# Kernel optimization log

Measured on AMD Instinct MI355X. Metric: run time of the kernel, lower is better.

Reference implementation:

```python
import jax, jax.numpy as jnp
import numpy as np
import itertools

EPS = 1e-5
SCALE = 16 ** -0.5  # key_dim ** -0.5
H_HEADS, KEY_DIM, D, RES, RES_, STRIDE = 8, 16, 32, 28, 14, 2


def hardswish(x):
    return x * jnp.clip(x + 3.0, 0.0, 6.0) / 6.0


def conv_bn_hw(x, w, g, b, m, v):
    # 1x1 conv (no bias) + eval-mode BatchNorm + Hardswish
    y = jnp.einsum('bchw,oc->bohw', x, w)
    scale = (g / jnp.sqrt(v + EPS))[:, None, None]
    y = (y - m[:, None, None]) * scale + b[:, None, None]
    return hardswish(y)


def _bias_idxs():
    offsets, idxs = {}, []
    for p1 in itertools.product(range(RES_), repeat=2):
        for p2 in itertools.product(range(RES), repeat=2):
            off = (abs(p1[0] * STRIDE - p2[0]), abs(p1[1] * STRIDE - p2[1]))
            if off not in offsets:
                offsets[off] = len(offsets)
            idxs.append(offsets[off])
    return np.array(idxs, dtype=np.int32).reshape(RES_ * RES_, RES * RES), len(offsets)


def setup_inputs() -> dict:
    key = jax.random.key(0)
    ks = jax.random.split(key, 8)
    B, C = 64, 256
    idxs, n_off = _bias_idxs()

    def bn_params(k, n):
        k1, k2, k3, k4 = jax.random.split(k, 4)
        return (jax.random.normal(k1, (n,)) * 0.1 + 1.0,
                jax.random.normal(k2, (n,)) * 0.1,
                jax.random.normal(k3, (n,)) * 0.1,
                jax.random.uniform(k4, (n,), minval=0.5, maxval=1.5))

    kv_g, kv_b, kv_m, kv_v = bn_params(ks[1], 384)
    q_g, q_b, q_m, q_v = bn_params(ks[2], 128)
    p_g, p_b, p_m, p_v = bn_params(ks[3], 512)
    return dict(
        x=jax.random.normal(ks[0], (B, C, 28, 28), dtype=jnp.float32),
        kv_w=jax.random.normal(ks[4], (384, C)) * 0.05,
        kv_g=kv_g, kv_b=kv_b, kv_m=kv_m, kv_v=kv_v,
        q_w=jax.random.normal(ks[5], (128, C)) * 0.05,
        q_g=q_g, q_b=q_b, q_m=q_m, q_v=q_v,
        proj_w=jax.random.normal(ks[6], (512, 256)) * 0.05,
        proj_g=p_g, proj_b=p_b, proj_m=p_m, proj_v=p_v,
        ab=jax.random.normal(ks[7], (H_HEADS, n_off)) * 0.02,
        bias_idxs=jnp.asarray(idxs),
    )


def reference(x, kv_w, kv_g, kv_b, kv_m, kv_v, q_w, q_g, q_b, q_m, q_v,
              proj_w, proj_g, proj_b, proj_m, proj_v, ab, bias_idxs):
    B = x.shape[0]
    N, N_ = RES * RES, RES_ * RES_
    kv = conv_bn_hw(x, kv_w, kv_g, kv_b, kv_m, kv_v).reshape(B, H_HEADS, KEY_DIM + D, N)
    k, v = kv[:, :, :KEY_DIM], kv[:, :, KEY_DIM:]
    # AvgPool2d(kernel=1, stride=2) == strided slice
    q = conv_bn_hw(x[:, :, ::STRIDE, ::STRIDE], q_w, q_g, q_b, q_m, q_v)
    q = q.reshape(B, H_HEADS, KEY_DIM, N_)
    bias = ab[:, bias_idxs]  # gather -> [H, N_, N]
    attn = jax.nn.softmax(jnp.einsum('bhdn,bhdm->bhnm', q, k) * SCALE + bias, axis=-1)
    out = jnp.einsum('bhdm,bhnm->bhdn', v, attn).reshape(B, H_HEADS * D, RES_, RES_)
    return conv_bn_hw(hardswish(out), proj_w, proj_g, proj_b, proj_m, proj_v)
```

## Files before the change

kernel.cpp:

```cpp
#include <hip/hip_runtime.h>
#include <cstddef>
#include <cstdint>


#define SCALE_ATTN2 0.36067376f
#define LOG2E 1.44269504f
#define BN_EPS 1e-5f

typedef short s8v __attribute__((ext_vector_type(8)));
typedef short s4v __attribute__((ext_vector_type(4)));
typedef float f4v __attribute__((ext_vector_type(4)));

__device__ __forceinline__ float hswish(float y) {
    float t = fminf(fmaxf(y + 3.0f, 0.0f), 6.0f);
    return y * t * (1.0f / 6.0f);
}
__device__ __forceinline__ unsigned short bf16_rn(float f) {
    unsigned u = __float_as_uint(f);
    unsigned r = (u + 0x7FFFu + ((u >> 16) & 1u)) >> 16;
    return (unsigned short)r;
}
__device__ __forceinline__ float bf16_to_f(unsigned short h) {
    return __uint_as_float(((unsigned)h) << 16);
}
__device__ __forceinline__ void gload_lds16(const void* gsrc, void* ldsdst) {
    __builtin_amdgcn_global_load_lds(
        (const __attribute__((address_space(1))) unsigned int*)gsrc,
        (__attribute__((address_space(3))) unsigned int*)ldsdst, 16, 0, 0);
}

__global__ __launch_bounds__(256)
void wprep(const float* __restrict__ W, short* __restrict__ hi,
           short* __restrict__ lo, int n4)
{
    int i = blockIdx.x * 256 + threadIdx.x;
    int stride = gridDim.x * 256;
    for (; i < n4; i += stride) {
        float4 v = reinterpret_cast<const float4*>(W)[i];
        s4v h, l;
        unsigned short hh;
        hh = bf16_rn(v.x); h[0] = (short)hh; l[0] = (short)bf16_rn(v.x - bf16_to_f(hh));
        hh = bf16_rn(v.y); h[1] = (short)hh; l[1] = (short)bf16_rn(v.y - bf16_to_f(hh));
        hh = bf16_rn(v.z); h[2] = (short)hh; l[2] = (short)bf16_rn(v.z - bf16_to_f(hh));
        hh = bf16_rn(v.w); h[3] = (short)hh; l[3] = (short)bf16_rn(v.w - bf16_to_f(hh));
        reinterpret_cast<s4v*>(hi)[i] = h;
        reinterpret_cast<s4v*>(lo)[i] = l;
    }
}

__global__ __launch_bounds__(256)
void xprep(const float* __restrict__ x, short* __restrict__ xT)
{
    __shared__ float T[64][65];
    int nt = blockIdx.x, b = blockIdx.y;
    int n0 = nt * 64;
    const float* xb = x + (size_t)b * 256 * 784;
    int t = threadIdx.x;
    int cr = t >> 2, s = t & 3;

    for (int ct = 0; ct < 4; ++ct) {
        __syncthreads();
#pragma unroll
        for (int qq = 0; qq < 4; ++qq) {
            int n = n0 + s * 16 + qq * 4;
            float4 v = make_float4(0.f, 0.f, 0.f, 0.f);
            if (n + 3 < 784)
                v = *reinterpret_cast<const float4*>(&xb[(size_t)(ct * 64 + cr) * 784 + n]);
            *reinterpret_cast<float4*>(&T[cr][s * 16 + qq * 4]) = v;
        }
        __syncthreads();
        int r = cr;
        if (n0 + r < 784) {
            size_t tb = ((((size_t)b * 13 + nt) * 4 + ct) << 13);
            short* hiB = xT + tb;
            short* loB = xT + tb + 4096;
            s8v h0, h1, l0, l1;
#pragma unroll
            for (int j = 0; j < 8; ++j) {
                float f = T[s * 16 + j][r];
                unsigned short hh = bf16_rn(f);
                h0[j] = (short)hh; l0[j] = (short)bf16_rn(f - bf16_to_f(hh));
            }
#pragma unroll
            for (int j = 0; j < 8; ++j) {
                float f = T[s * 16 + 8 + j][r];
                unsigned short hh = bf16_rn(f);
                h1[j] = (short)hh; l1[j] = (short)bf16_rn(f - bf16_to_f(hh));
            }
            int sw = (r & 7) << 3;
            int base = r * 64;
            *reinterpret_cast<s8v*>(&hiB[base + ((s * 16) ^ sw)]) = h0;
            *reinterpret_cast<s8v*>(&hiB[base + ((s * 16 + 8) ^ sw)]) = h1;
            *reinterpret_cast<s8v*>(&loB[base + ((s * 16) ^ sw)]) = l0;
            *reinterpret_cast<s8v*>(&loB[base + ((s * 16 + 8) ^ sw)]) = l1;
        }
    }
}

__global__ __launch_bounds__(256)
void bias_kernel(const float* __restrict__ ab, const int* __restrict__ idxs,
                 unsigned short* __restrict__ biasF, int n_off)
{
    int i = blockIdx.x * 256 + threadIdx.x;
    if (i < 196 * 784) {
        int id = idxs[i];
        int n = i / 784, m = i - n * 784;
#pragma unroll
        for (int h = 0; h < 8; ++h)
            biasF[((size_t)h * 208 + n) * 784 + m] = bf16_rn(ab[h * n_off + id] * LOG2E);
    }
}

__global__ __launch_bounds__(256)
void gemm_kv(const short* __restrict__ xT,
             const short* __restrict__ Whi, const short* __restrict__ Wlo,
             const float* __restrict__ G, const float* __restrict__ Bb,
             const float* __restrict__ Mm, const float* __restrict__ Vv,
             short* __restrict__ Kthi, short* __restrict__ Ktlo,
             short* __restrict__ Vbf)
{
    __shared__ short Bt[2][64][64];
    __shared__ float scs[128], shs[128];

    int nt = blockIdx.x, oy = blockIdx.y, b = blockIdx.z;
    int oBase = oy * 128;
    int tid = threadIdx.x, w = tid >> 6, l = tid & 63;
    int fr = l & 15, g = l >> 4;

    if (tid < 128) {
        int o = oBase + tid;
        float sc = G[o] * rsqrtf(Vv[o] + BN_EPS);
        scs[tid] = sc; shs[tid] = Bb[o] - Mm[o] * sc;
    }

    f4v acc[2][4];
#pragma unroll
    for (int i = 0; i < 2; ++i)
#pragma unroll
        for (int j = 0; j < 4; ++j) acc[i][j] = (f4v)0.0f;

    const char* tilesrc = (const char*)(xT) + ((((size_t)b * 13 + nt) * 4) << 14);
    char* ldsbase = (char*)&Bt[0][0][0];

    for (int ct = 0; ct < 4; ++ct) {
        __syncthreads();
        {
            const char* src = tilesrc + ((size_t)ct << 14) + w * 4096 + l * 16;
            char* dst = ldsbase + w * 4096;
#pragma unroll
            for (int j = 0; j < 4; ++j)
                gload_lds16(src + j * 1024, dst + j * 1024);
        }
        __syncthreads();
#pragma unroll
        for (int ks = 0; ks < 2; ++ks) {
            s8v ah[2], al[2];
#pragma unroll
            for (int mf = 0; mf < 2; ++mf) {
                int o = oBase + w * 32 + mf * 16 + fr;
                size_t wi = (size_t)o * 256 + ct * 64 + ks * 32 + g * 8;
                ah[mf] = *reinterpret_cast<const s8v*>(&Whi[wi]);
                al[mf] = *reinterpret_cast<const s8v*>(&Wlo[wi]);
            }
#pragma unroll
            for (int nf = 0; nf < 4; ++nf) {
                int r = nf * 16 + fr;
                int ci = (ks * 32 + g * 8) ^ ((r & 7) << 3);
                s8v bh = *reinterpret_cast<const s8v*>(&Bt[0][r][ci]);
                s8v bl = *reinterpret_cast<const s8v*>(&Bt[1][r][ci]);
#pragma unroll
                for (int mf = 0; mf < 2; ++mf) {
                    acc[mf][nf] = __builtin_amdgcn_mfma_f32_16x16x32_bf16(ah[mf], bh, acc[mf][nf], 0, 0, 0);
                    acc[mf][nf] = __builtin_amdgcn_mfma_f32_16x16x32_bf16(ah[mf], bl, acc[mf][nf], 0, 0, 0);
                    acc[mf][nf] = __builtin_amdgcn_mfma_f32_16x16x32_bf16(al[mf], bh, acc[mf][nf], 0, 0, 0);
                }
            }
        }
    }

    int nBase = nt * 64;
#pragma unroll
    for (int mf = 0; mf < 2; ++mf) {
        int ol = w * 32 + mf * 16 + g * 4;
        int o = oBase + ol;
        int h = o / 48;
        int c = o - h * 48;
        if (c < 16) {
#pragma unroll
            for (int nf = 0; nf < 4; ++nf) {
                int n = nBase + nf * 16 + fr;
                if (n < 784) {
                    s4v hv, lv;
#pragma unroll
                    for (int e = 0; e < 4; ++e) {
                        float z = hswish(acc[mf][nf][e] * scs[ol + e] + shs[ol + e]);
                        unsigned short hh = bf16_rn(z);
                        hv[e] = (short)hh; lv[e] = (short)bf16_rn(z - bf16_to_f(hh));
                    }
                    size_t ki = (((size_t)b * 8 + h) * 784 + n) * 16 + c;
                    *reinterpret_cast<s4v*>(&Kthi[ki]) = hv;
                    *reinterpret_cast<s4v*>(&Ktlo[ki]) = lv;
                }
            }
        } else {
            int d = c - 16;
#pragma unroll
            for (int nf = 0; nf < 4; ++nf) {
                int n = nBase + nf * 16 + fr;
                if (n < 784) {
#pragma unroll
                    for (int e = 0; e < 4; ++e) {
                        float z = hswish(acc[mf][nf][e] * scs[ol + e] + shs[ol + e]);
                        Vbf[(((size_t)b * 8 + h) * 32 + d + e) * 784 + n] = (short)bf16_rn(z);
                    }
                }
            }
        }
    }
}

__global__ __launch_bounds__(256)
void gemm_q(const float* __restrict__ x,
            const short* __restrict__ Whi, const short* __restrict__ Wlo,
            const float* __restrict__ G, const float* __restrict__ Bb,
            const float* __restrict__ Mm, const float* __restrict__ Vv,
            short* __restrict__ Qthi, short* __restrict__ Qtlo)
{
    __shared__ short Bt[2][64][64];
    __shared__ float scs[128], shs[128];

    int nt = blockIdx.x, b = blockIdx.z;
    const float* xb = x + (size_t)b * 256 * 784;
    int tid = threadIdx.x, w = tid >> 6, l = tid & 63;
    int fr = l & 15, g = l >> 4;
    int sr = tid >> 4, sc4 = (tid & 15) * 4;

    if (tid < 128) {
        int o = tid;
        float sc = G[o] * rsqrtf(Vv[o] + BN_EPS);
        scs[tid] = sc; shs[tid] = Bb[o] - Mm[o] * sc;
    }

    f4v acc[2][4];
#pragma unroll
    for (int i = 0; i < 2; ++i)
#pragma unroll
        for (int j = 0; j < 4; ++j) acc[i][j] = (f4v)0.0f;

    for (int ct = 0; ct < 4; ++ct) {
        __syncthreads();
#pragma unroll
        for (int jc = 0; jc < 4; ++jc) {
            int c = sr + jc * 16;
#pragma unroll
            for (int e = 0; e < 4; ++e) {
                int nn = nt * 64 + sc4 + e;
                float v = 0.0f;
                if (nn < 196) {
                    int rr = nn / 14, cc = nn - rr * 14;
                    v = xb[(size_t)(ct * 64 + c) * 784 + rr * 56 + cc * 2];
                }
                int r = sc4 + e;
                int ci = c ^ ((r & 7) << 3);
                unsigned short hh = bf16_rn(v);
                Bt[0][r][ci] = (short)hh;
                Bt[1][r][ci] = (short)bf16_rn(v - bf16_to_f(hh));
            }
        }
        __syncthreads();
#pragma unroll
        for (int ks = 0; ks < 2; ++ks) {
            s8v ah[2], al[2];
#pragma unroll
            for (int mf = 0; mf < 2; ++mf) {
                int o = w * 32 + mf * 16 + fr;
                size_t wi = (size_t)o * 256 + ct * 64 + ks * 32 + g * 8;
                ah[mf] = *reinterpret_cast<const s8v*>(&Whi[wi]);
                al[mf] = *reinterpret_cast<const s8v*>(&Wlo[wi]);
            }
#pragma unroll
            for (int nf = 0; nf < 4; ++nf) {
                int r = nf * 16 + fr;
                int ci = (ks * 32 + g * 8) ^ ((r & 7) << 3);
                s8v bh = *reinterpret_cast<const s8v*>(&Bt[0][r][ci]);
                s8v bl = *reinterpret_cast<const s8v*>(&Bt[1][r][ci]);
#pragma unroll
                for (int mf = 0; mf < 2; ++mf) {
                    acc[mf][nf] = __builtin_amdgcn_mfma_f32_16x16x32_bf16(ah[mf], bh, acc[mf][nf], 0, 0, 0);
                    acc[mf][nf] = __builtin_amdgcn_mfma_f32_16x16x32_bf16(ah[mf], bl, acc[mf][nf], 0, 0, 0);
                    acc[mf][nf] = __builtin_amdgcn_mfma_f32_16x16x32_bf16(al[mf], bh, acc[mf][nf], 0, 0, 0);
                }
            }
        }
    }

#pragma unroll
    for (int mf = 0; mf < 2; ++mf) {
        int ol = w * 32 + mf * 16 + g * 4;
        int h = ol >> 4, d0 = ol & 15;
#pragma unroll
        for (int nf = 0; nf < 4; ++nf) {
            int n = nt * 64 + nf * 16 + fr;
            if (n < 196) {
                s4v hv, lv;
#pragma unroll
                for (int e = 0; e < 4; ++e) {
                    float z = hswish(acc[mf][nf][e] * scs[ol + e] + shs[ol + e]);
                    unsigned short hh = bf16_rn(z);
                    hv[e] = (short)hh; lv[e] = (short)bf16_rn(z - bf16_to_f(hh));
                }
                size_t qi = (((size_t)b * 8 + h) * 196 + n) * 16 + d0;
                *reinterpret_cast<s4v*>(&Qthi[qi]) = hv;
                *reinterpret_cast<s4v*>(&Qtlo[qi]) = lv;
            }
        }
    }
}

__global__ __launch_bounds__(256, 8)
void attn_mfma(const short* __restrict__ Kthi, const short* __restrict__ Ktlo,
               const short* __restrict__ Vbf,
               const short* __restrict__ Qthi, const short* __restrict__ Qtlo,
               const unsigned short* __restrict__ biasF, short* __restrict__ actT)
{
    __shared__ short Pl[4][16][72];

    int tid = threadIdx.x, w = tid >> 6, l = tid & 63;
    int idx = blockIdx.x * 4 + w;
    int bh = idx / 13, tile = idx - bh * 13;
    int b = bh >> 3, h = bh & 7;
    int g = l >> 4, fr = l & 15;

    const short* Kbase = ((g < 2) ? Kthi : Ktlo) + (size_t)bh * 784 * 16;
    const short* Vb = Vbf + (size_t)bh * 32 * 784;
    const short* Qh = Qthi + (size_t)bh * 196 * 16;
    const short* Ql = Qtlo + (size_t)bh * 196 * 16;
    int n = tile * 16 + fr;
    const unsigned short* bB = biasF + ((size_t)h * 208 + n) * 784;

    s8v qf1 = (s8v)0, qf2 = (s8v)0;
    if (n < 196) {
        qf1 = *reinterpret_cast<const s8v*>(&Qh[(size_t)n * 16 + (g & 1) * 8]);
        if (g < 2) qf2 = *reinterpret_cast<const s8v*>(&Ql[(size_t)n * 16 + g * 8]);
    }

    f4v Oa0 = (f4v)0.0f, Oa1 = (f4v)0.0f;
    float M = -1e30f, L = 0.0f;

#pragma unroll 1
    for (int ch = 0; ch < 13; ++ch) {
        int m0 = ch * 64;
        int subLim = (ch == 12) ? 1 : 4;
        int mlim = (ch == 12) ? 16 : 64;

        float s[4][4];
#pragma unroll
        for (int sub = 0; sub < 4; ++sub) {
            if (sub < subLim) {
                int mg = m0 + sub * 16 + fr;
                s8v af = *reinterpret_cast<const s8v*>(&Kbase[(size_t)mg * 16 + (g & 1) * 8]);
                f4v a = (f4v)0.0f;
                a = __builtin_amdgcn_mfma_f32_16x16x32_bf16(af, qf1, a, 0, 0, 0);
                a = __builtin_amdgcn_mfma_f32_16x16x32_bf16(af, qf2, a, 0, 0, 0);
                s4v bv = *reinterpret_cast<const s4v*>(&bB[m0 + sub * 16 + g * 4]);
#pragma unroll
                for (int e = 0; e < 4; ++e)
                    s[sub][e] = a[e] * SCALE_ATTN2 + bf16_to_f((unsigned short)bv[e]);
            } else {
#pragma unroll
                for (int e = 0; e < 4; ++e) s[sub][e] = -1e30f;
            }
        }

        float mx = fmaxf(fmaxf(fmaxf(s[0][0], s[0][1]), fmaxf(s[0][2], s[0][3])),
                         fmaxf(fmaxf(s[1][0], s[1][1]), fmaxf(s[1][2], s[1][3])));
        mx = fmaxf(mx, fmaxf(fmaxf(fmaxf(s[2][0], s[2][1]), fmaxf(s[2][2], s[2][3])),
                             fmaxf(fmaxf(s[3][0], s[3][1]), fmaxf(s[3][2], s[3][3]))));
        mx = fmaxf(mx, __shfl_xor(mx, 16));
        mx = fmaxf(mx, __shfl_xor(mx, 32));
        if (__any(mx > M + 8.0f)) {
            float Mn = fmaxf(M, mx);
            float corr = exp2f(M - Mn);
            L *= corr;
#pragma unroll
            for (int e = 0; e < 4; ++e) { Oa0[e] *= corr; Oa1[e] *= corr; }
            M = Mn;
        }

        float Ls = 0.0f;
#pragma unroll
        for (int sub = 0; sub < 4; ++sub) {
            float p[4];
#pragma unroll
            for (int e = 0; e < 4; ++e) {
                int mml = sub * 16 + g * 4 + e;
                float pv = exp2f(s[sub][e] - M);
                p[e] = (mml < mlim) ? pv : 0.0f;
                Ls += p[e];
            }
            unsigned w0, w1;
            asm("v_cvt_pk_bf16_f32 %0, %1, %2" : "=v"(w0) : "v"(p[0]), "v"(p[1]));
            asm("v_cvt_pk_bf16_f32 %0, %1, %2" : "=v"(w1) : "v"(p[2]), "v"(p[3]));
            int mb = sub * 16 + g * 4;
            *reinterpret_cast<unsigned*>(&Pl[w][fr][mb]) = w0;
            *reinterpret_cast<unsigned*>(&Pl[w][fr][mb + 2]) = w1;
        }
        Ls += __shfl_xor(Ls, 16);
        Ls += __shfl_xor(Ls, 32);
        L += Ls;

#pragma unroll
        for (int kc = 0; kc < 2; ++kc) {
            s8v pf = *reinterpret_cast<const s8v*>(&Pl[w][fr][kc * 32 + g * 8]);
            int mf0 = m0 + kc * 32 + g * 8;
            s8v v0 = (s8v)0, v1 = (s8v)0;
            if (mf0 + 8 <= 784) {
                v0 = *reinterpret_cast<const s8v*>(&Vb[(size_t)fr * 784 + mf0]);
                v1 = *reinterpret_cast<const s8v*>(&Vb[(size_t)(16 + fr) * 784 + mf0]);
            }
            Oa0 = __builtin_amdgcn_mfma_f32_16x16x32_bf16(v0, pf, Oa0, 0, 0, 0);
            Oa1 = __builtin_amdgcn_mfma_f32_16x16x32_bf16(v1, pf, Oa1, 0, 0, 0);
        }
    }

    if (n < 196) {
        float inv = 1.0f / L;
        int r = n & 63, ntl = n >> 6;
        int sw = (r & 7) << 3;
#pragma unroll
        for (int dt = 0; dt < 2; ++dt) {
            int c0 = h * 32 + dt * 16 + g * 4;
            f4v* Op = dt ? &Oa1 : &Oa0;
            s4v hv, lv;
#pragma unroll
            for (int e = 0; e < 4; ++e) {
                float z = hswish((*Op)[e] * inv);
                unsigned short hh = bf16_rn(z);
                hv[e] = (short)hh; lv[e] = (short)bf16_rn(z - bf16_to_f(hh));
            }
            int ct = c0 >> 6, c2 = c0 & 63;
            size_t tb = ((((size_t)b * 4 + ntl) * 4 + ct) << 13);
            int idx2 = r * 64 + (c2 ^ sw);
            *reinterpret_cast<s4v*>(&actT[tb + idx2]) = hv;
            *reinterpret_cast<s4v*>(&actT[tb + 4096 + idx2]) = lv;
        }
    }
}

__global__ __launch_bounds__(256)
void gemm_proj(const short* __restrict__ actT,
               const short* __restrict__ Whi, const short* __restrict__ Wlo,
               const float* __restrict__ G, const float* __restrict__ Bb,
               const float* __restrict__ Mm, const float* __restrict__ Vv,
               float* __restrict__ out)
{
    __shared__ short Bt[2][64][64];
    __shared__ float scs[128], shs[128];

    int nt = blockIdx.x, oy = blockIdx.y, b = blockIdx.z;
    int oBase = oy * 128;
    int tid = threadIdx.x, w = tid >> 6, l = tid & 63;
    int fr = l & 15, g = l >> 4;

    if (tid < 128) {
        int o = oBase + tid;
        float sc = G[o] * rsqrtf(Vv[o] + BN_EPS);
        scs[tid] = sc; shs[tid] = Bb[o] - Mm[o] * sc;
    }

    f4v acc[2][4];
#pragma unroll
    for (int i = 0; i < 2; ++i)
#pragma unroll
        for (int j = 0; j < 4; ++j) acc[i][j] = (f4v)0.0f;

    const char* tilesrc = (const char*)(actT) + ((((size_t)b * 4 + nt) * 4) << 14);
    char* ldsbase = (char*)&Bt[0][0][0];

    for (int ct = 0; ct < 4; ++ct) {
        __syncthreads();
        {
            const char* src = tilesrc + ((size_t)ct << 14) + w * 4096 + l * 16;
            char* dst = ldsbase + w * 4096;
#pragma unroll
            for (int j = 0; j < 4; ++j)
                gload_lds16(src + j * 1024, dst + j * 1024);
        }
        __syncthreads();
#pragma unroll
        for (int ks = 0; ks < 2; ++ks) {
            s8v ah[2], al[2];
#pragma unroll
            for (int mf = 0; mf < 2; ++mf) {
                int o = oBase + w * 32 + mf * 16 + fr;
                size_t wi = (size_t)o * 256 + ct * 64 + ks * 32 + g * 8;
                ah[mf] = *reinterpret_cast<const s8v*>(&Whi[wi]);
                al[mf] = *reinterpret_cast<const s8v*>(&Wlo[wi]);
            }
#pragma unroll
            for (int nf = 0; nf < 4; ++nf) {
                int r = nf * 16 + fr;
                int ci = (ks * 32 + g * 8) ^ ((r & 7) << 3);
                s8v bh = *reinterpret_cast<const s8v*>(&Bt[0][r][ci]);
                s8v bl = *reinterpret_cast<const s8v*>(&Bt[1][r][ci]);
#pragma unroll
                for (int mf = 0; mf < 2; ++mf) {
                    acc[mf][nf] = __builtin_amdgcn_mfma_f32_16x16x32_bf16(ah[mf], bh, acc[mf][nf], 0, 0, 0);
                    acc[mf][nf] = __builtin_amdgcn_mfma_f32_16x16x32_bf16(ah[mf], bl, acc[mf][nf], 0, 0, 0);
                    acc[mf][nf] = __builtin_amdgcn_mfma_f32_16x16x32_bf16(al[mf], bh, acc[mf][nf], 0, 0, 0);
                }
            }
        }
    }

#pragma unroll
    for (int mf = 0; mf < 2; ++mf) {
        int ol = w * 32 + mf * 16 + g * 4;
#pragma unroll
        for (int nf = 0; nf < 4; ++nf) {
            int n = nt * 64 + nf * 16 + fr;
            if (n < 196) {
#pragma unroll
                for (int e = 0; e < 4; ++e) {
                    float z = hswish(acc[mf][nf][e] * scs[ol + e] + shs[ol + e]);
                    out[((size_t)b * 512 + oBase + ol + e) * 196 + n] = z;
                }
            }
        }
    }
}

extern "C" void kernel_launch(void* const* d_in, const int* in_sizes, int n_in,
                              void* d_out, int out_size, void* d_ws, size_t ws_size,
                              hipStream_t stream) {
    const float* x      = (const float*)d_in[0];
    const float* kv_w   = (const float*)d_in[1];
    const float* kv_g   = (const float*)d_in[2];
    const float* kv_b   = (const float*)d_in[3];
    const float* kv_m   = (const float*)d_in[4];
    const float* kv_v   = (const float*)d_in[5];
    const float* q_w    = (const float*)d_in[6];
    const float* q_g    = (const float*)d_in[7];
    const float* q_b    = (const float*)d_in[8];
    const float* q_m    = (const float*)d_in[9];
    const float* q_v    = (const float*)d_in[10];
    const float* proj_w = (const float*)d_in[11];
    const float* proj_g = (const float*)d_in[12];
    const float* proj_b = (const float*)d_in[13];
    const float* proj_m = (const float*)d_in[14];
    const float* proj_v = (const float*)d_in[15];
    const float* ab     = (const float*)d_in[16];
    const int*   idxs   = (const int*)d_in[17];
    float* out = (float*)d_out;

    int n_off = in_sizes[16] / 8;

    char* p = (char*)d_ws;
    size_t off = 0;
    auto alloc = [&](size_t bytes) -> char* {
        char* r = p + off;
        off += (bytes + 255) & ~(size_t)255;
        return r;
    };
    short* Kthi = (short*)alloc((size_t)64 * 8 * 784 * 16 * 2);
    short* Ktlo = (short*)alloc((size_t)64 * 8 * 784 * 16 * 2);
    short* Vbf  = (short*)alloc((size_t)64 * 8 * 32 * 784 * 2);
    short* Qthi = (short*)alloc((size_t)64 * 8 * 196 * 16 * 2);
    short* Qtlo = (short*)alloc((size_t)64 * 8 * 196 * 16 * 2);
    unsigned short* biasF = (unsigned short*)alloc((size_t)8 * 208 * 784 * 2);
    short* Wkvh = (short*)alloc((size_t)384 * 256 * 2);
    short* Wkvl = (short*)alloc((size_t)384 * 256 * 2);
    short* Wqh  = (short*)alloc((size_t)128 * 256 * 2);
    short* Wql  = (short*)alloc((size_t)128 * 256 * 2);
    short* Wpjh = (short*)alloc((size_t)512 * 256 * 2);
    short* Wpjl = (short*)alloc((size_t)512 * 256 * 2);
    short* xT   = (short*)alloc((size_t)64 * 13 * 4 * 16384);
    short* actT = xT;

    wprep<<<dim3(64), 256, 0, stream>>>(kv_w, Wkvh, Wkvl, 384 * 256 / 4);
    wprep<<<dim3(64), 256, 0, stream>>>(q_w, Wqh, Wql, 128 * 256 / 4);
    wprep<<<dim3(64), 256, 0, stream>>>(proj_w, Wpjh, Wpjl, 512 * 256 / 4);
    xprep<<<dim3(13, 64), 256, 0, stream>>>(x, xT);
    bias_kernel<<<dim3((196 * 784 + 255) / 256), 256, 0, stream>>>(ab, idxs, biasF, n_off);
    gemm_kv<<<dim3(13, 3, 64), 256, 0, stream>>>(xT, Wkvh, Wkvl, kv_g, kv_b, kv_m, kv_v,
                                                 Kthi, Ktlo, Vbf);
    gemm_q<<<dim3(4, 1, 64), 256, 0, stream>>>(x, Wqh, Wql, q_g, q_b, q_m, q_v,
                                               Qthi, Qtlo);
    attn_mfma<<<dim3(512 * 13 / 4), 256, 0, stream>>>(Kthi, Ktlo, Vbf, Qthi, Qtlo, biasF, actT);
    gemm_proj<<<dim3(4, 4, 64), 256, 0, stream>>>(actT, Wpjh, Wpjl,
                                                  proj_g, proj_b, proj_m, proj_v, out);
}
```

Measured before the change: 387.7 us.

## Widen GEMM output tiles, merge weight prep, zero-pad bias, remap attention blocks

gemm_kv now computes all 384 output channels per block and gemm_proj computes 256 per block. Each staged LDS tile of the activations is therefore reused across more output rows, and there are fewer blocks that reload the same x tile. The three weight-prep launches are merged into one kernel. The bias kernel now zero-fills the padded rows. The attention grid index is permuted so neighbouring blocks spread across heads or XCDs, and the softmax max reduction is rewritten as a loop. The wider accumulators raise register pressure and cut the number of blocks, which risks lower occupancy.

Result: slower. 409.1 us (+5.5%).

```diff
diff --git a/kernel.cpp b/kernel.cpp
--- a/kernel.cpp
+++ b/kernel.cpp
@@ -30,21 +30,29 @@
 }
 
 __global__ __launch_bounds__(256)
-void wprep(const float* __restrict__ W, short* __restrict__ hi,
-           short* __restrict__ lo, int n4)
+void wprep_all(const float* __restrict__ kvw, const float* __restrict__ qw,
+               const float* __restrict__ pjw,
+               short* __restrict__ kvh, short* __restrict__ kvl,
+               short* __restrict__ qh, short* __restrict__ ql,
+               short* __restrict__ pjh, short* __restrict__ pjl)
 {
+    const int n0 = 384 * 256 / 4, n1 = 128 * 256 / 4, n2 = 512 * 256 / 4;
     int i = blockIdx.x * 256 + threadIdx.x;
     int stride = gridDim.x * 256;
-    for (; i < n4; i += stride) {
-        float4 v = reinterpret_cast<const float4*>(W)[i];
+    for (; i < n0 + n1 + n2; i += stride) {
+        const float* W; short *hi, *lo; int j;
+        if (i < n0)           { W = kvw; hi = kvh; lo = kvl; j = i; }
+        else if (i < n0 + n1) { W = qw;  hi = qh;  lo = ql;  j = i - n0; }
+        else                  { W = pjw; hi = pjh; lo = pjl; j = i - n0 - n1; }
+        float4 v = reinterpret_cast<const float4*>(W)[j];
         s4v h, l;
         unsigned short hh;
         hh = bf16_rn(v.x); h[0] = (short)hh; l[0] = (short)bf16_rn(v.x - bf16_to_f(hh));
         hh = bf16_rn(v.y); h[1] = (short)hh; l[1] = (short)bf16_rn(v.y - bf16_to_f(hh));
         hh = bf16_rn(v.z); h[2] = (short)hh; l[2] = (short)bf16_rn(v.z - bf16_to_f(hh));
         hh = bf16_rn(v.w); h[3] = (short)hh; l[3] = (short)bf16_rn(v.w - bf16_to_f(hh));
-        reinterpret_cast<s4v*>(hi)[i] = h;
-        reinterpret_cast<s4v*>(lo)[i] = l;
+        reinterpret_cast<s4v*>(hi)[j] = h;
+        reinterpret_cast<s4v*>(lo)[j] = l;
     }
 }
 
@@ -102,12 +110,18 @@
                  unsigned short* __restrict__ biasF, int n_off)
 {
     int i = blockIdx.x * 256 + threadIdx.x;
-    if (i < 196 * 784) {
-        int id = idxs[i];
+    if (i < 208 * 784) {
         int n = i / 784, m = i - n * 784;
-#pragma unroll
-        for (int h = 0; h < 8; ++h)
-            biasF[((size_t)h * 208 + n) * 784 + m] = bf16_rn(ab[h * n_off + id] * LOG2E);
+        if (n < 196) {
+            int id = idxs[i];
+#pragma unroll
+            for (int h = 0; h < 8; ++h)
+                biasF[((size_t)h * 208 + n) * 784 + m] = bf16_rn(ab[h * n_off + id] * LOG2E);
+        } else {
+#pragma unroll
+            for (int h = 0; h < 8; ++h)
+                biasF[((size_t)h * 208 + n) * 784 + m] = 0;
+        }
     }
 }
 
@@ -120,24 +134,24 @@
              short* __restrict__ Vbf)
 {
     __shared__ short Bt[2][64][64];
-    __shared__ float scs[128], shs[128];
-
-    int nt = blockIdx.x, oy = blockIdx.y, b = blockIdx.z;
-    int oBase = oy * 128;
+    __shared__ float scs[384], shs[384];
+
+    int nt = blockIdx.x, b = blockIdx.y;
     int tid = threadIdx.x, w = tid >> 6, l = tid & 63;
     int fr = l & 15, g = l >> 4;
 
-    if (tid < 128) {
-        int o = oBase + tid;
-        float sc = G[o] * rsqrtf(Vv[o] + BN_EPS);
-        scs[tid] = sc; shs[tid] = Bb[o] - Mm[o] * sc;
-    }
-
-    f4v acc[2][4];
-#pragma unroll
-    for (int i = 0; i < 2; ++i)
-#pragma unroll
-        for (int j = 0; j < 4; ++j) acc[i][j] = (f4v)0.0f;
+    for (int r = tid; r < 384; r += 256) {
+        float sc = G[r] * rsqrtf(Vv[r] + BN_EPS);
+        scs[r] = sc; shs[r] = Bb[r] - Mm[r] * sc;
+    }
+
+    f4v acc[3][2][4];
+#pragma unroll
+    for (int oy = 0; oy < 3; ++oy)
+#pragma unroll
+        for (int i = 0; i < 2; ++i)
+#pragma unroll
+            for (int j = 0; j < 4; ++j) acc[oy][i][j] = (f4v)0.0f;
 
     const char* tilesrc = (const char*)(xT) + ((((size_t)b * 13 + nt) * 4) << 14);
     char* ldsbase = (char*)&Bt[0][0][0];
@@ -154,37 +168,44 @@
         __syncthreads();
 #pragma unroll
         for (int ks = 0; ks < 2; ++ks) {
-            s8v ah[2], al[2];
-#pragma unroll
-            for (int mf = 0; mf < 2; ++mf) {
-                int o = oBase + w * 32 + mf * 16 + fr;
-                size_t wi = (size_t)o * 256 + ct * 64 + ks * 32 + g * 8;
-                ah[mf] = *reinterpret_cast<const s8v*>(&Whi[wi]);
-                al[mf] = *reinterpret_cast<const s8v*>(&Wlo[wi]);
-            }
+            s8v bh[4], bl[4];
 #pragma unroll
             for (int nf = 0; nf < 4; ++nf) {
                 int r = nf * 16 + fr;
                 int ci = (ks * 32 + g * 8) ^ ((r & 7) << 3);
-                s8v bh = *reinterpret_cast<const s8v*>(&Bt[0][r][ci]);
-                s8v bl = *reinterpret_cast<const s8v*>(&Bt[1][r][ci]);
+                bh[nf] = *reinterpret_cast<const s8v*>(&Bt[0][r][ci]);
+                bl[nf] = *reinterpret_cast<const s8v*>(&Bt[1][r][ci]);
+            }
+#pragma unroll
+            for (int oy = 0; oy < 3; ++oy) {
+                s8v ah[2], al[2];
 #pragma unroll
                 for (int mf = 0; mf < 2; ++mf) {
-                    acc[mf][nf] = __builtin_amdgcn_mfma_f32_16x16x32_bf16(ah[mf], bh, acc[mf][nf], 0, 0, 0);
-                    acc[mf][nf] = __builtin_amdgcn_mfma_f32_16x16x32_bf16(ah[mf], bl, acc[mf][nf], 0, 0, 0);
-                    acc[mf][nf] = __builtin_amdgcn_mfma_f32_16x16x32_bf16(al[mf], bh, acc[mf][nf], 0, 0, 0);
-                }
+                    int o = oy * 128 + w * 32 + mf * 16 + fr;
+                    size_t wi = (size_t)o * 256 + ct * 64 + ks * 32 + g * 8;
+                    ah[mf] = *reinterpret_cast<const s8v*>(&Whi[wi]);
+                    al[mf] = *reinterpret_cast<const s8v*>(&Wlo[wi]);
+                }
+#pragma unroll
+                for (int nf = 0; nf < 4; ++nf)
+#pragma unroll
+                    for (int mf = 0; mf < 2; ++mf) {
+                        acc[oy][mf][nf] = __builtin_amdgcn_mfma_f32_16x16x32_bf16(ah[mf], bh[nf], acc[oy][mf][nf], 0, 0, 0);
+                        acc[oy][mf][nf] = __builtin_amdgcn_mfma_f32_16x16x32_bf16(ah[mf], bl[nf], acc[oy][mf][nf], 0, 0, 0);
+                        acc[oy][mf][nf] = __builtin_amdgcn_mfma_f32_16x16x32_bf16(al[mf], bh[nf], acc[oy][mf][nf], 0, 0, 0);
+                    }
             }
         }
     }
 
     int nBase = nt * 64;
 #pragma unroll
+    for (int oy = 0; oy < 3; ++oy)
+#pragma unroll
     for (int mf = 0; mf < 2; ++mf) {
-        int ol = w * 32 + mf * 16 + g * 4;
-        int o = oBase + ol;
-        int h = o / 48;
-        int c = o - h * 48;
+        int ol = oy * 128 + w * 32 + mf * 16 + g * 4;
+        int h = ol / 48;
+        int c = ol - h * 48;
         if (c < 16) {
 #pragma unroll
             for (int nf = 0; nf < 4; ++nf) {
@@ -193,7 +214,7 @@
                     s4v hv, lv;
 #pragma unroll
                     for (int e = 0; e < 4; ++e) {
-                        float z = hswish(acc[mf][nf][e] * scs[ol + e] + shs[ol + e]);
+                        float z = hswish(acc[oy][mf][nf][e] * scs[ol + e] + shs[ol + e]);
                         unsigned short hh = bf16_rn(z);
                         hv[e] = (short)hh; lv[e] = (short)bf16_rn(z - bf16_to_f(hh));
                     }
@@ -210,7 +231,7 @@
                 if (n < 784) {
 #pragma unroll
                     for (int e = 0; e < 4; ++e) {
-                        float z = hswish(acc[mf][nf][e] * scs[ol + e] + shs[ol + e]);
+                        float z = hswish(acc[oy][mf][nf][e] * scs[ol + e] + shs[ol + e]);
                         Vbf[(((size_t)b * 8 + h) * 32 + d + e) * 784 + n] = (short)bf16_rn(z);
                     }
                 }
@@ -326,7 +347,8 @@
     __shared__ short Pl[4][16][72];
 
     int tid = threadIdx.x, w = tid >> 6, l = tid & 63;
-    int idx = blockIdx.x * 4 + w;
+    int lb = (blockIdx.x & 7) * 208 + (blockIdx.x >> 3);
+    int idx = lb * 4 + w;
     int bh = idx / 13, tile = idx - bh * 13;
     int b = bh >> 3, h = bh & 7;
     int g = l >> 4, fr = l & 15;
@@ -372,10 +394,11 @@
             }
         }
 
-        float mx = fmaxf(fmaxf(fmaxf(s[0][0], s[0][1]), fmaxf(s[0][2], s[0][3])),
-                         fmaxf(fmaxf(s[1][0], s[1][1]), fmaxf(s[1][2], s[1][3])));
-        mx = fmaxf(mx, fmaxf(fmaxf(fmaxf(s[2][0], s[2][1]), fmaxf(s[2][2], s[2][3])),
-                             fmaxf(fmaxf(s[3][0], s[3][1]), fmaxf(s[3][2], s[3][3]))));
+        float mx = s[0][0];
+#pragma unroll
+        for (int sub = 0; sub < 4; ++sub)
+#pragma unroll
+            for (int e = 0; e < 4; ++e) mx = fmaxf(mx, s[sub][e]);
         mx = fmaxf(mx, __shfl_xor(mx, 16));
         mx = fmaxf(mx, __shfl_xor(mx, 32));
         if (__any(mx > M + 8.0f)) {
@@ -430,11 +453,11 @@
 #pragma unroll
         for (int dt = 0; dt < 2; ++dt) {
             int c0 = h * 32 + dt * 16 + g * 4;
-            f4v* Op = dt ? &Oa1 : &Oa0;
+            f4v Ov = dt ? Oa1 : Oa0;
             s4v hv, lv;
 #pragma unroll
             for (int e = 0; e < 4; ++e) {
-                float z = hswish((*Op)[e] * inv);
+                float z = hswish(Ov[e] * inv);
                 unsigned short hh = bf16_rn(z);
                 hv[e] = (short)hh; lv[e] = (short)bf16_rn(z - bf16_to_f(hh));
             }
@@ -455,24 +478,26 @@
                float* __restrict__ out)
 {
     __shared__ short Bt[2][64][64];
-    __shared__ float scs[128], shs[128];
-
-    int nt = blockIdx.x, oy = blockIdx.y, b = blockIdx.z;
-    int oBase = oy * 128;
+    __shared__ float scs[256], shs[256];
+
+    int nt = blockIdx.x, oy2 = blockIdx.y, b = blockIdx.z;
+    int oBase = oy2 * 256;
     int tid = threadIdx.x, w = tid >> 6, l = tid & 63;
     int fr = l & 15, g = l >> 4;
 
-    if (tid < 128) {
+    {
         int o = oBase + tid;
         float sc = G[o] * rsqrtf(Vv[o] + BN_EPS);
         scs[tid] = sc; shs[tid] = Bb[o] - Mm[o] * sc;
     }
 
-    f4v acc[2][4];
-#pragma unroll
-    for (int i = 0; i < 2; ++i)
-#pragma unroll
-        for (int j = 0; j < 4; ++j) acc[i][j] = (f4v)0.0f;
+    f4v acc[2][2][4];
+#pragma unroll
+    for (int oz = 0; oz < 2; ++oz)
+#pragma unroll
+        for (int i = 0; i < 2; ++i)
+#pragma unroll
+            for (int j = 0; j < 4; ++j) acc[oz][i][j] = (f4v)0.0f;
 
     const char* tilesrc = (const char*)(actT) + ((((size_t)b * 4 + nt) * 4) << 14);
     char* ldsbase = (char*)&Bt[0][0][0];
@@ -489,40 +514,48 @@
         __syncthreads();
 #pragma unroll
         for (int ks = 0; ks < 2; ++ks) {
-            s8v ah[2], al[2];
-#pragma unroll
-            for (int mf = 0; mf < 2; ++mf) {
-                int o = oBase + w * 32 + mf * 16 + fr;
-                size_t wi = (size_t)o * 256 + ct * 64 + ks * 32 + g * 8;
-                ah[mf] = *reinterpret_cast<const s8v*>(&Whi[wi]);
-                al[mf] = *reinterpret_cast<const s8v*>(&Wlo[wi]);
-            }
+            s8v bh[4], bl[4];
 #pragma unroll
             for (int nf = 0; nf < 4; ++nf) {
                 int r = nf * 16 + fr;
                 int ci = (ks * 32 + g * 8) ^ ((r & 7) << 3);
-                s8v bh = *reinterpret_cast<const s8v*>(&Bt[0][r][ci]);
-                s8v bl = *reinterpret_cast<const s8v*>(&Bt[1][r][ci]);
+                bh[nf] = *reinterpret_cast<const s8v*>(&Bt[0][r][ci]);
+                bl[nf] = *reinterpret_cast<const s8v*>(&Bt[1][r][ci]);
+            }
+#pragma unroll
+            for (int oz = 0; oz < 2; ++oz) {
+                s8v ah[2], al[2];
 #pragma unroll
                 for (int mf = 0; mf < 2; ++mf) {
-                    acc[mf][nf] = __builtin_amdgcn_mfma_f32_16x16x32_bf16(ah[mf], bh, acc[mf][nf], 0, 0, 0);
-                    acc[mf][nf] = __builtin_amdgcn_mfma_f32_16x16x32_bf16(ah[mf], bl, acc[mf][nf], 0, 0, 0);
-                    acc[mf][nf] = __builtin_amdgcn_mfma_f32_16x16x32_bf16(al[mf], bh, acc[mf][nf], 0, 0, 0);
-                }
-            }
-        }
-    }
-
+                    int o = oBase + oz * 128 + w * 32 + mf * 16 + fr;
+                    size_t wi = (size_t)o * 256 + ct * 64 + ks * 32 + g * 8;
+                    ah[mf] = *reinterpret_cast<const s8v*>(&Whi[wi]);
+                    al[mf] = *reinterpret_cast<const s8v*>(&Wlo[wi]);
+                }
+#pragma unroll
+                for (int nf = 0; nf < 4; ++nf)
+#pragma unroll
+                    for (int mf = 0; mf < 2; ++mf) {
+                        acc[oz][mf][nf] = __builtin_amdgcn_mfma_f32_16x16x32_bf16(ah[mf], bh[nf], acc[oz][mf][nf], 0, 0, 0);
+                        acc[oz][mf][nf] = __builtin_amdgcn_mfma_f32_16x16x32_bf16(ah[mf], bl[nf], acc[oz][mf][nf], 0, 0, 0);
+                        acc[oz][mf][nf] = __builtin_amdgcn_mfma_f32_16x16x32_bf16(al[mf], bh[nf], acc[oz][mf][nf], 0, 0, 0);
+                    }
+            }
+        }
+    }
+
+#pragma unroll
+    for (int oz = 0; oz < 2; ++oz)
 #pragma unroll
     for (int mf = 0; mf < 2; ++mf) {
-        int ol = w * 32 + mf * 16 + g * 4;
+        int ol = oz * 128 + w * 32 + mf * 16 + g * 4;
 #pragma unroll
         for (int nf = 0; nf < 4; ++nf) {
             int n = nt * 64 + nf * 16 + fr;
             if (n < 196) {
 #pragma unroll
                 for (int e = 0; e < 4; ++e) {
-                    float z = hswish(acc[mf][nf][e] * scs[ol + e] + shs[ol + e]);
+                    float z = hswish(acc[oz][mf][nf][e] * scs[ol + e] + shs[ol + e]);
                     out[((size_t)b * 512 + oBase + ol + e) * 196 + n] = z;
                 }
             }
@@ -577,16 +610,15 @@
     short* xT   = (short*)alloc((size_t)64 * 13 * 4 * 16384);
     short* actT = xT;
 
-    wprep<<<dim3(64), 256, 0, stream>>>(kv_w, Wkvh, Wkvl, 384 * 256 / 4);
-    wprep<<<dim3(64), 256, 0, stream>>>(q_w, Wqh, Wql, 128 * 256 / 4);
-    wprep<<<dim3(64), 256, 0, stream>>>(proj_w, Wpjh, Wpjl, 512 * 256 / 4);
+    wprep_all<<<dim3(64), 256, 0, stream>>>(kv_w, q_w, proj_w,
+                                            Wkvh, Wkvl, Wqh, Wql, Wpjh, Wpjl);
     xprep<<<dim3(13, 64), 256, 0, stream>>>(x, xT);
-    bias_kernel<<<dim3((196 * 784 + 255) / 256), 256, 0, stream>>>(ab, idxs, biasF, n_off);
-    gemm_kv<<<dim3(13, 3, 64), 256, 0, stream>>>(xT, Wkvh, Wkvl, kv_g, kv_b, kv_m, kv_v,
-                                                 Kthi, Ktlo, Vbf);
+    bias_kernel<<<dim3((208 * 784 + 255) / 256), 256, 0, stream>>>(ab, idxs, biasF, n_off);
+    gemm_kv<<<dim3(13, 64), 256, 0, stream>>>(xT, Wkvh, Wkvl, kv_g, kv_b, kv_m, kv_v,
+                                              Kthi, Ktlo, Vbf);
     gemm_q<<<dim3(4, 1, 64), 256, 0, stream>>>(x, Wqh, Wql, q_g, q_b, q_m, q_v,
                                                Qthi, Qtlo);
-    attn_mfma<<<dim3(512 * 13 / 4), 256, 0, stream>>>(Kthi, Ktlo, Vbf, Qthi, Qtlo, biasF, actT);
-    gemm_proj<<<dim3(4, 4, 64), 256, 0, stream>>>(actT, Wpjh, Wpjl,
+    attn_mfma<<<dim3(1664), 256, 0, stream>>>(Kthi, Ktlo, Vbf, Qthi, Qtlo, biasF, actT);
+    gemm_proj<<<dim3(4, 2, 64), 256, 0, stream>>>(actT, Wpjh, Wpjl,
                                                   proj_g, proj_b, proj_m, proj_v, out);
 }
```
